# Performance work log

Hardware: AMD Instinct MI355X
Metric: run time of the kernel (lower is better)

## Reference

```python
import jax, jax.numpy as jnp
import numpy as np

N = 512           # nodes
DIM = 64          # feature dim (in_dim == dim)
KS = (0.9, 0.7, 0.6)
M_DIM = 17
EDGE_DIM = 1
EIN = 2 * DIM + 1 + EDGE_DIM  # EGNN edge-mlp input width = 130
L = 3             # shared EGNN layers per scale


def _rn(k, shape, s=0.05):
    return jax.random.normal(k, shape, jnp.float32) * s


def setup_inputs() -> dict:
    key = jax.random.key(0)
    k = jax.random.split(key, 12)
    feat = jax.random.normal(k[0], (1, N, DIM), jnp.float32)
    coor = jax.random.normal(k[1], (1, N, 3), jnp.float32)
    # sparse-ish binary adjacency stored densely, as the module expects
    edge = (jax.random.uniform(k[2], (1, N, N, 1)) < 0.05).astype(jnp.float32)
    return {
        "feat": feat, "coor": coor, "edge": edge,
        "We1": _rn(k[3], (L, EIN, 2 * EIN)), "be1": jnp.zeros((L, 2 * EIN), jnp.float32),
        "We2": _rn(k[4], (L, 2 * EIN, M_DIM)), "be2": jnp.zeros((L, M_DIM), jnp.float32),
        "Wc1": _rn(k[5], (L, M_DIM, 4 * M_DIM)), "bc1": jnp.zeros((L, 4 * M_DIM), jnp.float32),
        "Wc2": _rn(k[6], (L, 4 * M_DIM, 1)), "bc2": jnp.zeros((L, 1), jnp.float32),
        "Wn1": _rn(k[7], (L, DIM + M_DIM, 2 * DIM)), "bn1": jnp.zeros((L, 2 * DIM), jnp.float32),
        "Wn2": _rn(k[8], (L, 2 * DIM, DIM)), "bn2": jnp.zeros((L, DIM), jnp.float32),
        "wp": _rn(k[9], (len(KS), DIM)), "bp": jnp.zeros((len(KS),), jnp.float32),
        "ep": 0,
    }


def _egnn(feats, coors, edges, We1, be1, We2, be2, Wc1, bc1, Wc2, bc2,
          Wn1, bn1, Wn2, bn2):
    # feats [B,n,d], coors [B,n,3], edges [B,n,n,1]
    rel = coors[:, :, None, :] - coors[:, None, :, :]           # [B,n,n,3]
    dist = jnp.sum(rel * rel, axis=-1, keepdims=True)           # [B,n,n,1]
    B, n, d = feats.shape
    fi = jnp.broadcast_to(feats[:, :, None, :], (B, n, n, d))
    fj = jnp.broadcast_to(feats[:, None, :, :], (B, n, n, d))
    e_in = jnp.concatenate([fi, fj, dist, edges], axis=-1)      # [B,n,n,EIN]
    m = jax.nn.silu(jax.nn.silu(e_in @ We1 + be1) @ We2 + be2)  # [B,n,n,M]
    cw = jax.nn.silu(m @ Wc1 + bc1) @ Wc2 + bc2                 # [B,n,n,1]
    coors_out = coors + jnp.sum(cw * rel, axis=2)               # [B,n,3]
    m_i = jnp.sum(m, axis=2)                                    # [B,n,M]
    h = jax.nn.silu(jnp.concatenate([feats, m_i], axis=-1) @ Wn1 + bn1) @ Wn2 + bn2
    return feats + h, coors_out


def _forward(feat, coor, edge, We1, be1, We2, be2, Wc1, bc1, Wc2, bc2,
             Wn1, bn1, Wn2, bn2, wp, bp):
    org_h, org_g, org_c = feat[0], edge[0, :, :, 0], coor[0]
    n_nodes = org_h.shape[0]
    ug = (org_g != 0).astype(jnp.float32)
    ug2 = ((ug @ ug) != 0).astype(jnp.float32)  # 2-hop closure adjacency
    hs = []
    for i, kf in enumerate(KS):
        kcnt = max(2, int(kf * n_nodes))
        scores = jax.nn.sigmoid(org_h @ wp[i] + bp[i])          # [n]
        vals, idx = jax.lax.top_k(scores, kcnt)
        h = org_h[idx] * vals[:, None]                          # gather + scale
        g = ug2[idx][:, idx]                                    # row+col gather
        c = org_c[idx]
        hc, coors, edges = h[None], c[None], g[None, :, :, None]
        for j in range(3):
            ht, coors = _egnn(hc, coors, edges,
                              We1[j], be1[j], We2[j], be2[j],
                              Wc1[j], bc1[j], Wc2[j], bc2[j],
                              Wn1[j], bn1[j], Wn2[j], bn2[j])
            hc = jax.nn.relu(hc + ht)
        # unpool: zero-scatter back to original node set
        h_full = jnp.zeros((n_nodes, hc.shape[-1]), hc.dtype).at[idx].set(hc[0])
        hs.append(h_full)
    out = hs[-1]
    for h_i in hs:
        out = jnp.maximum(out, h_i)
    return out


def reference(feat, coor, edge, We1, be1, We2, be2, Wc1, bc1, Wc2, bc2,
              Wn1, bn1, Wn2, bn2, wp, bp, ep):
    return _forward(feat, coor, edge, We1, be1, We2, be2, Wc1, bc1, Wc2, bc2,
                    Wn1, bn1, Wn2, bn2, wp, bp)
```

## Files before the change

### kernel.cpp

```cpp
#include <hip/hip_runtime.h>
#include <hip/hip_bf16.h>

typedef unsigned long long u64;
typedef unsigned int u32;
typedef unsigned short u16;

#define NN   512
#define DIMF 64
#define E2   260
#define KPAD 272
#define MD   17
#define MH   68
#define NH1  128
#define K0   460
#define K1   358
#define K2   307
#define KT   1125
#define O1   460
#define O2   818
#define PADU 1152
#define AS   272
#define NT0  8
#define NT1  6
#define NT2  5
#define T0T   (K0*NT0)
#define T01T  (T0T + K1*NT1)
#define TTOT  (T01T + K2*NT2)
#define PBLK  ((TTOT+3)/4)
#define MSTR  40
#define WVLDS 5120

#define KNEG  (-1.4426950408889634f)
#define LN2N  (-0.6931471805599453f)

typedef __attribute__((ext_vector_type(8)))  short short8;
typedef __attribute__((ext_vector_type(16))) float f32x16;

union SF  { int4 i4; u16 us[8]; u32 w[4]; short8 v; };
union F4U { float4 v; float2 h[2]; float f[4]; u32 w[4]; };

__device__ __forceinline__ float fast_exp2(float x){
#if __has_builtin(__builtin_amdgcn_exp2f)
    return __builtin_amdgcn_exp2f(x);
#else
    return __expf(x * 0.6931471805599453f);
#endif
}
__device__ __forceinline__ float fast_rcp(float x){
#if __has_builtin(__builtin_amdgcn_rcpf)
    return __builtin_amdgcn_rcpf(x);
#else
    return __fdividef(1.0f, x);
#endif
}
__device__ __forceinline__ float silups(float q){
    return q * fast_rcp(1.0f + fast_exp2(q));
}
__device__ __forceinline__ float sigf(float x){
    return fast_rcp(1.0f + fast_exp2(x * KNEG));
}
__device__ __forceinline__ u16 bf16_rne(float f){
    u32 u = __float_as_uint(f);
    u += 0x7FFFu + ((u >> 16) & 1u);
    return (u16)(u >> 16);
}
__device__ __forceinline__ float bf16f(u16 h){
    return __uint_as_float(((u32)h) << 16);
}
__device__ __forceinline__ u32 pk_bf16(float x, float y){
    float2 f2; f2.x = x; f2.y = y;
    __hip_bfloat162 h = __float22bfloat162_rn(f2);
    union { __hip_bfloat162 b; u32 u; } cv; cv.b = h;
    return cv.u;
}
__device__ __forceinline__ void lgkm_wait(){
#if __has_builtin(__builtin_amdgcn_s_waitcnt)
    __builtin_amdgcn_s_waitcnt(0xC07F);
#endif
}
__device__ __forceinline__ float2 f2add(float2 a, float2 b){ return float2{a.x+b.x, a.y+b.y}; }
__device__ __forceinline__ float2 f2mul(float2 a, float2 b){ return float2{a.x*b.x, a.y*b.y}; }
__device__ __forceinline__ float2 f2fma(float2 a, float2 b, float2 c){
    return float2{fmaf(a.x,b.x,c.x), fmaf(a.y,b.y,c.y)};
}
__device__ __forceinline__ float2 sig2s(float2 q){
    float ex = fast_exp2(q.x), ey = fast_exp2(q.y);
    float2 den = f2add(float2{1.0f, 1.0f}, float2{ex, ey});
    float2 r; r.x = fast_rcp(den.x); r.y = fast_rcp(den.y);
    return f2mul(q, r);
}

__global__ __launch_bounds__(256) void k_pre(
    const float* __restrict__ edge, const float* __restrict__ feat,
    const float* __restrict__ wp, const float* __restrict__ bp,
    const float* __restrict__ We2, const float* __restrict__ Wc1,
    const float* __restrict__ We1, const float* __restrict__ be2,
    const float* __restrict__ bc1, const float* __restrict__ Wc2,
    u64* __restrict__ ugw, float* __restrict__ scores,
    u16* __restrict__ W2f, u16* __restrict__ Wc1f,
    float* __restrict__ wdP, float* __restrict__ weP, float* __restrict__ be2P,
    float* __restrict__ bc1P, float* __restrict__ Wc2P, u64* __restrict__ ug2w){
    int blk = blockIdx.x, t = threadIdx.x;
    if (blk < 128){
        int i = blk*4 + (t>>6); int lane = t&63;
        const float* row = edge + (size_t)i*NN;
        for (int w = 0; w < 8; w++){
            u64 m = __ballot(row[w*64+lane] != 0.0f);
            if (lane == 0) ugw[i*8+w] = m;
        }
        return;
    }
    if (blk < 134){
        int gid = (blk-128)*256 + t; if (gid >= 3*NN) return;
        int l = gid>>9, n = gid&511;
        const float4* fr = (const float4*)(feat + n*DIMF);
        const float4* wr = (const float4*)(wp + l*DIMF);
        float s = bp[l];
        for (int d = 0; d < 16; d++){
            float4 f = fr[d], w = wr[d];
            s = fmaf(f.x, w.x, s); s = fmaf(f.y, w.y, s);
            s = fmaf(f.z, w.z, s); s = fmaf(f.w, w.w, s);
        }
        scores[gid] = sigf(s);
        return;
    }
    int idx = (blk-134)*256 + t;
    if (idx < 52224){
        int e = idx&7, lane = (idx>>3)&63, hl = (idx>>9)&1, c = (idx>>10)%17, jl = idx/17408;
        int q = lane>>5, nn = lane&31;
        int k = c*16 + q*8 + e;
        float v = (k < E2 && nn < MD) ? We2[jl*E2*MD + k*MD + nn] : 0.0f;
        u16 hi = bf16_rne(v);
        W2f[idx] = hl ? bf16_rne(v - bf16f(hi)) : hi;
        return;
    }
    idx -= 52224;
    if (idx < 9216){
        int e = idx & 7, lane = (idx>>3)&63, c2 = (idx>>9)&1, T = (idx>>10)%3, jl = idx/3072;
        int q = lane>>5, nn = lane&31;
        int o = c2*16 + q*8 + e, h = T*32 + nn;
        float v = (o < MD && h < MH) ? Wc1[jl*MD*MH + o*MH + h] : 0.0f;
        Wc1f[idx] = bf16_rne(v);
        return;
    }
    idx -= 9216;
    if (idx < 816){ int jl = idx/KPAD, k = idx%KPAD;
        wdP[idx] = (k < E2) ? We1[jl*130*E2 + 128*E2 + k]*KNEG : 0.0f; return; }
    idx -= 816;
    if (idx < 816){ int jl = idx/KPAD, k = idx%KPAD;
        weP[idx] = (k < E2) ? We1[jl*130*E2 + 129*E2 + k]*KNEG : 0.0f; return; }
    idx -= 816;
    if (idx < 96){ int jl = idx/32, o = idx%32;
        be2P[idx] = (o < MD) ? be2[jl*MD+o]*KNEG : 0.0f; return; }
    idx -= 96;
    if (idx < 288){ int jl = idx/96, h = idx%96;
        bc1P[idx] = (h < MH) ? bc1[jl*MH+h]*KNEG : 0.0f; return; }
    idx -= 288;
    if (idx < 288){ int jl = idx/96, h = idx%96;
        Wc2P[idx] = (h < MH) ? Wc2[jl*MH+h]*LN2N : 0.0f; return; }
    idx -= 288;
    if (idx < 4096){ ug2w[idx] = 0ULL; return; }
}

__global__ __launch_bounds__(512) void k_sortug2(
    const float* __restrict__ scores, const u64* __restrict__ ugw,
    float* __restrict__ svals, int* __restrict__ sidx, int* __restrict__ rev,
    u64* __restrict__ ug2w){
    int blk = blockIdx.x, t = threadIdx.x;
    if (blk < 3){
        int l = blk;
        __shared__ float sk[NN];
        __shared__ int   si[NN];
        float key = scores[l*NN+t]; int idx = t;
        rev[l*NN+t] = -1;
        for (int k = 2; k <= NN; k <<= 1){
            for (int jj = k>>1; jj > 0; jj >>= 1){
                float kb; int ib;
                if (jj >= 64){
                    sk[t] = key; si[t] = idx;
                    __syncthreads();
                    kb = sk[t^jj]; ib = si[t^jj];
                    __syncthreads();
                } else {
                    kb = __shfl_xor(key, jj);
                    ib = __shfl_xor(idx, jj);
                }
                bool aFirst = (key > kb) || (key == kb && idx < ib);
                bool down   = ((t & k) == 0);
                bool lower  = ((t & jj) == 0);
                bool keep   = (aFirst == (lower == down));
                key = keep ? key : kb;
                idx = keep ? idx : ib;
            }
        }
        svals[l*NN+t] = key; sidx[l*NN+t] = idx;
        int kcnt = (l==0)?K0:(l==1)?K1:K2;
        if (t < kcnt) rev[l*NN + idx] = t;
    } else {
        int gid = (blk-3)*512 + t;
        int i  = gid >> 6;
        int w  = (gid >> 3) & 7;
        int kc = gid & 7;
        u64 rm = ugw[i*8 + kc];
        u64 acc = 0;
        int base = kc*64;
        while (rm){
            int k2 = __builtin_ctzll(rm);
            rm &= rm - 1;
            acc |= ugw[(base + k2)*8 + w];
        }
        if (acc) atomicOr(&ug2w[i*8 + w], acc);
    }
}

__device__ __forceinline__ void ab_comp(int jl, const float* __restrict__ We1,
                                        const float* __restrict__ be1, float hval,
                                        int u, int lane,
                                        float* __restrict__ Ap, float* __restrict__ BF){
    const float* W = We1 + jl*130*E2;
    int r  = 4*lane;
    int rt = 256 + lane;
    int rtc = (lane < 4) ? rt : 256;
    F4U av; av.v = *(const float4*)(be1 + jl*E2 + r);
    F4U bv; bv.f[0]=bv.f[1]=bv.f[2]=bv.f[3]=0.0f;
    float avx = be1[jl*E2 + rtc];
    float bvx = 0.0f;
    for (int d = 0; d < DIMF; d++){
        float hv = __shfl(hval, d);
        F4U w1; w1.v = *(const float4*)(W + d*E2 + r);
        F4U w2; w2.v = *(const float4*)(W + (DIMF+d)*E2 + r);
#pragma unroll
        for (int i = 0; i < 4; i++){
            av.f[i] = fmaf(hv, w1.f[i], av.f[i]);
            bv.f[i] = fmaf(hv, w2.f[i], bv.f[i]);
        }
        avx = fmaf(hv, W[d*E2 + rtc], avx);
        bvx = fmaf(hv, W[(DIMF+d)*E2 + rtc], bvx);
    }
#pragma unroll
    for (int i = 0; i < 4; i++){ av.f[i] *= KNEG; bv.f[i] *= KNEG; }
    avx *= KNEG; bvx *= KNEG;
    *(float4*)(Ap + u*AS + r) = av.v;
    *(float4*)(BF + ((size_t)(lane>>1)*PADU + u)*8 + (lane&1)*4) = bv.v;
    if (lane < 16){
        int k = 256 + lane;
        float aval = (lane < 4) ? avx : 0.0f;
        float bval = (lane < 4) ? bvx : 0.0f;
        Ap[u*AS + k] = aval;
        BF[((size_t)(k>>3)*PADU + u)*8 + (k&7)] = bval;
    }
}

__global__ __launch_bounds__(256) void k_gab(
    const float* __restrict__ feat, const float* __restrict__ coor,
    const float* __restrict__ svals, const int* __restrict__ sidx,
    const float* __restrict__ We1, const float* __restrict__ be1,
    float* __restrict__ hc, float* __restrict__ c0, float* __restrict__ c1,
    float* __restrict__ mi, float* __restrict__ Ap, float* __restrict__ BF){
    int t = threadIdx.x; int u = blockIdx.x*4 + (t>>6); if (u >= KT) return;
    int lane = t&63;
    int l = (u<K0)?0:(u<O2)?1:2;
    int a = u - ((l==0)?0:(l==1)?O1:O2);
    int org = sidx[l*NN+a];
    float val = svals[l*NN+a];
    float hval = feat[org*DIMF+lane]*val;
    hc[u*DIMF+lane] = hval;
    if (lane < 3){ float c = coor[org*3+lane]; c0[u*4+lane]=c; c1[u*4+lane]=c; }
    if (lane == 3){ c0[u*4+3]=0.0f; c1[u*4+3]=0.0f; }
    if (lane < 20) mi[u*20+lane] = 0.0f;
    ab_comp(0, We1, be1, hval, u, lane, Ap, BF);
}

template<int DOCW>
__global__ __launch_bounds__(256, 4) void k_pair(
    int jl,
    const float* __restrict__ Ap, const float* __restrict__ BF,
    const u16* __restrict__ W2f, const u16* __restrict__ Wc1f,
    const float* __restrict__ wdP, const float* __restrict__ weP,
    const float* __restrict__ be2P, const float* __restrict__ bc1P,
    const float* __restrict__ Wc2P, const float* __restrict__ bc2,
    const float* __restrict__ cin, float* __restrict__ cout,
    float* __restrict__ mi, const int* __restrict__ sidx,
    const u64* __restrict__ ug2w){
    __shared__ __align__(16) char sWK[4*WVLDS];
    __shared__ __align__(16) char sWD[1088];
    __shared__ __align__(16) char sWE[1088];
    int t = threadIdx.x;
    if (t < 68)       ((float4*)sWD)[t]    = *(const float4*)(wdP + jl*KPAD + 4*t);
    else if (t < 136) ((float4*)sWE)[t-68] = *(const float4*)(weP + jl*KPAD + 4*(t-68));
    int wid0 = blockIdx.x*4 + (t>>6);
    int lane = t&63, n = lane&31, q = lane>>5;
    bool dead = (wid0 >= TTOT);
    int wid = dead ? (TTOT-1) : wid0;
    int l, kl, off, a, tile;
    if (wid < T0T)       { l=0; kl=K0; off=0;  a = wid>>3; tile = wid&7; }
    else if (wid < T01T) { int w = wid-T0T;  l=1; kl=K1; off=O1; a = w/NT1; tile = w - a*NT1; }
    else                 { int w = wid-T01T; l=2; kl=K2; off=O2; a = w/NT2; tile = w - a*NT2; }
    int u = off + a;
    int b0 = tile*64 + n, b1 = b0 + 32;
    float act0 = (b0 < kl) ? 1.0f : 0.0f;
    float act1 = (b1 < kl) ? 1.0f : 0.0f;
    int b0c = min(b0, kl-1), b1c = min(b1, kl-1);
    int ub0 = off + b0c, ub1 = off + b1c;
    int ia  = sidx[l*NN+a];
    int ib0 = sidx[l*NN+b0c], ib1 = sidx[l*NN+b1c];
    float ef0 = act0 * (float)((ug2w[ia*8 + (ib0>>6)] >> (ib0&63)) & 1ULL);
    float ef1 = act1 * (float)((ug2w[ia*8 + (ib1>>6)] >> (ib1&63)) & 1ULL);
    F4U ca;  ca.v  = ((const float4*)cin)[u];
    F4U cb0; cb0.v = ((const float4*)cin)[ub0];
    F4U cb1; cb1.v = ((const float4*)cin)[ub1];
    float tx0 = ca.f[0]-cb0.f[0], ty0 = ca.f[1]-cb0.f[1], tz0 = ca.f[2]-cb0.f[2];
    float tx1 = ca.f[0]-cb1.f[0], ty1 = ca.f[1]-cb1.f[1], tz1 = ca.f[2]-cb1.f[2];
    float dd0 = tx0*tx0 + ty0*ty0 + tz0*tz0;
    float dd1 = tx1*tx1 + ty1*ty1 + tz1*tz1;

    char* myk = sWK + (t>>6)*WVLDS;
    {
        const float* Au = Ap + u*AS;
        ((float4*)myk)[lane] = *(const float4*)(Au + 4*lane);
        if (lane < 4) ((float4*)myk)[64+lane] = *(const float4*)(Au + 256 + 4*lane);
    }
    __syncthreads();

    const float* pB0 = BF + ((size_t)q*PADU + ub0)*8;
    const float* pB1 = BF + ((size_t)q*PADU + ub1)*8;
    const u16*   pW  = W2f + jl*17408 + lane*8;
    const char*  pA  = myk + q*32;
    const char*  pWD = sWD + q*32;
    const char*  pWE = sWE + q*32;

    f32x16 acc0, acc1;
#pragma unroll
    for (int r = 0; r < 16; r++){ acc0[r] = 0.0f; acc1[r] = 0.0f; }

    F4U nb0a, nb0b, nb1a, nb1b; SF nwh;
    nb0a.v = *(const float4*)(pB0);     nb0b.v = *(const float4*)(pB0 + 4);
    nb1a.v = *(const float4*)(pB1);     nb1b.v = *(const float4*)(pB1 + 4);
    nwh.i4 = *(const int4*)(pW);

    float2 DD0{dd0,dd0}, EF0{ef0,ef0}, DD1{dd1,dd1}, EF1{ef1,ef1};

    for (int c = 0; c < 17; c++){
        F4U b0a = nb0a, b0b = nb0b, b1a = nb1a, b1b = nb1b;
        SF  wh  = nwh;
        pB0 += 2*PADU*8; pB1 += 2*PADU*8; pW += 1024;
        if (c < 16){
            nb0a.v = *(const float4*)(pB0);     nb0b.v = *(const float4*)(pB0 + 4);
            nb1a.v = *(const float4*)(pB1);     nb1b.v = *(const float4*)(pB1 + 4);
            nwh.i4 = *(const int4*)(pW);
        }
        F4U a0, a1, w0, w1, e0, e1;
        a0.v = *(const float4*)(pA);       a1.v = *(const float4*)(pA + 16);
        w0.v = *(const float4*)(pWD);      w1.v = *(const float4*)(pWD + 16);
        e0.v = *(const float4*)(pWE);      e1.v = *(const float4*)(pWE + 16);
        pA += 64; pWD += 64; pWE += 64;

        SF shi0, shi1;
#pragma unroll
        for (int h = 0; h < 2; h++){
            float2 p00 = f2fma(EF0, e0.h[h], f2fma(DD0, w0.h[h], f2add(a0.h[h], b0a.h[h])));
            float2 p01 = f2fma(EF0, e1.h[h], f2fma(DD0, w1.h[h], f2add(a1.h[h], b0b.h[h])));
            float2 p10 = f2fma(EF1, e0.h[h], f2fma(DD1, w0.h[h], f2add(a0.h[h], b1a.h[h])));
            float2 p11 = f2fma(EF1, e1.h[h], f2fma(DD1, w1.h[h], f2add(a1.h[h], b1b.h[h])));
            float2 s00 = sig2s(p00), s01 = sig2s(p01);
            float2 s10 = sig2s(p10), s11 = sig2s(p11);
            shi0.w[h]   = pk_bf16(s00.x, s00.y);
            shi0.w[2+h] = pk_bf16(s01.x, s01.y);
            shi1.w[h]   = pk_bf16(s10.x, s10.y);
            shi1.w[2+h] = pk_bf16(s11.x, s11.y);
        }
        acc0 = __builtin_amdgcn_mfma_f32_32x32x16_bf16(shi0.v, wh.v, acc0, 0, 0, 0);
        acc1 = __builtin_amdgcn_mfma_f32_32x32x16_bf16(shi1.v, wh.v, acc1, 0, 0, 0);
    }

    float be2v = be2P[jl*32 + n];
    u16* mlds = (u16*)myk;
    float msum = 0.0f;
#pragma unroll
    for (int r = 0; r < 16; r++){
        int row = (r&3) + 8*(r>>2) + 4*q;
        float m0 = silups(acc0[r] + be2v);
        float m1 = silups(acc1[r] + be2v);
        m0 = (tile*64 + row      < kl) ? m0 : 0.0f;
        m1 = (tile*64 + 32 + row < kl) ? m1 : 0.0f;
        msum += m0 + m1;
        if (DOCW){
            mlds[row*MSTR + n]        = bf16_rne(m0);
            mlds[(row+32)*MSTR + n]   = bf16_rne(m1);
        }
    }
    msum += __shfl_xor(msum, 32);
    if (!dead && lane < MD) atomicAdd(&mi[u*20 + lane], msum * LN2N);

    if (DOCW){
        lgkm_wait();
        const char* mb = (const char*)mlds;
        float gx = 0.0f, gy = 0.0f, gz = 0.0f;
        float bc2v = bc2[jl];
#pragma unroll
        for (int S = 0; S < 2; S++){
            SF af0, af1;
            af0.i4 = *(const int4*)(mb + (S*32+n)*(MSTR*2) + q*16);
            af1.i4 = *(const int4*)(mb + (S*32+n)*(MSTR*2) + 32 + q*16);
            float cwp[16];
#pragma unroll
            for (int r = 0; r < 16; r++) cwp[r] = 0.0f;
            for (int T = 0; T < 3; T++){
                SF bb0, bb1;
                bb0.i4 = *(const int4*)(Wc1f + jl*3072 + T*1024 +       lane*8);
                bb1.i4 = *(const int4*)(Wc1f + jl*3072 + T*1024 + 512 + lane*8);
                f32x16 p2;
#pragma unroll
                for (int r = 0; r < 16; r++) p2[r] = 0.0f;
                p2 = __builtin_amdgcn_mfma_f32_32x32x16_bf16(af0.v, bb0.v, p2, 0, 0, 0);
                p2 = __builtin_amdgcn_mfma_f32_32x32x16_bf16(af1.v, bb1.v, p2, 0, 0, 0);
                float bc1v = bc1P[jl*96 + T*32 + n];
                float wc2v = Wc2P[jl*96 + T*32 + n];
#pragma unroll
                for (int r = 0; r < 16; r++)
                    cwp[r] = fmaf(silups(p2[r] + bc1v), wc2v, cwp[r]);
            }
#pragma unroll
            for (int r = 0; r < 16; r++){
                int row  = (r&3) + 8*(r>>2) + 4*q + S*32;
                int brow = tile*64 + row;
                F4U cbr; cbr.v = ((const float4*)cin)[off + min(brow, kl-1)];
                float cw = cwp[r] + ((n == 0) ? bc2v : 0.0f);
                cw = (brow < kl) ? cw : 0.0f;
                gx = fmaf(cw, ca.f[0]-cbr.f[0], gx);
                gy = fmaf(cw, ca.f[1]-cbr.f[1], gy);
                gz = fmaf(cw, ca.f[2]-cbr.f[2], gz);
            }
        }
#pragma unroll
        for (int s = 1; s < 64; s <<= 1){
            gx += __shfl_xor(gx, s); gy += __shfl_xor(gy, s); gz += __shfl_xor(gz, s);
        }
        if (!dead && lane == 0){
            atomicAdd(&cout[u*4+0], gx);
            atomicAdd(&cout[u*4+1], gy);
            atomicAdd(&cout[u*4+2], gz);
        }
    }
}

__global__ __launch_bounds__(256) void k_nodeab(
    int jl, int donext, int docopy,
    const float* __restrict__ Wn1, const float* __restrict__ bn1,
    const float* __restrict__ Wn2, const float* __restrict__ bn2,
    const float* __restrict__ We1, const float* __restrict__ be1,
    float* __restrict__ hc, float* __restrict__ mi,
    const float* __restrict__ ccur, float* __restrict__ cnext,
    float* __restrict__ Ap, float* __restrict__ BF){
    int t = threadIdx.x; int u = blockIdx.x*4 + (t>>6); if (u >= KT) return;
    int lane = t&63;
    float hval = hc[u*DIMF+lane];
    float mval = (lane < MD) ? mi[u*20+lane] : 0.0f;
    const float* W1 = Wn1 + jl*(DIMF+MD)*NH1;
    float v0 = bn1[jl*NH1+lane], v1 = bn1[jl*NH1+lane+64];
    for (int d = 0; d < DIMF; d++){
        float x = __shfl(hval, d);
        v0 = fmaf(x, W1[d*NH1+lane],    v0);
        v1 = fmaf(x, W1[d*NH1+lane+64], v1);
    }
    for (int d = 0; d < MD; d++){
        float x = __shfl(mval, d);
        v0 = fmaf(x, W1[(DIMF+d)*NH1+lane],    v0);
        v1 = fmaf(x, W1[(DIMF+d)*NH1+lane+64], v1);
    }
    float s0 = silups(v0 * KNEG) * LN2N, s1 = silups(v1 * KNEG) * LN2N;
    const float* W2 = Wn2 + jl*NH1*DIMF;
    float h = bn2[jl*DIMF+lane];
    for (int i = 0; i < 64; i++) h = fmaf(__shfl(s0, i), W2[i*DIMF+lane], h);
    for (int i = 0; i < 64; i++) h = fmaf(__shfl(s1, i), W2[(64+i)*DIMF+lane], h);
    float hn = fmaxf(0.0f, fmaf(2.0f, hval, h));
    hc[u*DIMF+lane] = hn;
    if (donext){
        if (lane < 20) mi[u*20+lane] = 0.0f;
        if (docopy && lane < 4) cnext[u*4+lane] = ccur[u*4+lane];
        ab_comp(jl+1, We1, be1, hn, u, lane, Ap, BF);
    }
}

__global__ void k_final(const float* __restrict__ hc, const int* __restrict__ rev,
                        float* __restrict__ out){
    int gid = blockIdx.x*blockDim.x + threadIdx.x;
    if (gid >= NN*DIMF) return;
    int nn = gid>>6, d = gid&63;
    float v = 0.0f;
    int a0 = rev[0*NN+nn]; if (a0 >= 0) v = fmaxf(v, hc[(0  + a0)*DIMF + d]);
    int a1 = rev[1*NN+nn]; if (a1 >= 0) v = fmaxf(v, hc[(O1 + a1)*DIMF + d]);
    int a2 = rev[2*NN+nn]; if (a2 >= 0) v = fmaxf(v, hc[(O2 + a2)*DIMF + d]);
    out[gid] = v;
}

extern "C" void kernel_launch(void* const* d_in, const int* in_sizes, int n_in,
                              void* d_out, int out_size, void* d_ws, size_t ws_size,
                              hipStream_t stream) {
    (void)in_sizes; (void)n_in; (void)out_size; (void)ws_size;
    const float* feat = (const float*)d_in[0];
    const float* coor = (const float*)d_in[1];
    const float* edge = (const float*)d_in[2];
    const float* We1  = (const float*)d_in[3];
    const float* be1  = (const float*)d_in[4];
    const float* We2  = (const float*)d_in[5];
    const float* be2  = (const float*)d_in[6];
    const float* Wc1  = (const float*)d_in[7];
    const float* bc1  = (const float*)d_in[8];
    const float* Wc2  = (const float*)d_in[9];
    const float* bc2  = (const float*)d_in[10];
    const float* Wn1  = (const float*)d_in[11];
    const float* bn1  = (const float*)d_in[12];
    const float* Wn2  = (const float*)d_in[13];
    const float* bn2  = (const float*)d_in[14];
    const float* wp   = (const float*)d_in[15];
    const float* bp   = (const float*)d_in[16];
    float* out = (float*)d_out;

    char* wsb = (char*)d_ws;
    u64*   ugw    = (u64*)  (wsb + 0);
    u64*   ug2w   = (u64*)  (wsb + 32768);
    float* scores = (float*)(wsb + 65536);
    float* svals  = (float*)(wsb + 71680);
    int*   sidx   = (int*)  (wsb + 77824);
    int*   rev    = (int*)  (wsb + 83968);
    float* c0     = (float*)(wsb + 90112);
    float* c1     = (float*)(wsb + 108544);
    float* mi     = (float*)(wsb + 126976);
    float* hc     = (float*)(wsb + 217088);
    float* Ap     = (float*)(wsb + 505344);
    float* BF     = (float*)(wsb + 1729536);
    u16*   W2f    = (u16*)  (wsb + 2982912);
    u16*   Wc1f   = (u16*)  (wsb + 3087360);
    float* wdP    = (float*)(wsb + 3105792);
    float* weP    = (float*)(wsb + 3109120);
    float* be2P   = (float*)(wsb + 3112448);
    float* bc1P   = (float*)(wsb + 3112832);
    float* Wc2P   = (float*)(wsb + 3113984);

    k_pre<<<399, 256, 0, stream>>>(edge, feat, wp, bp, We2, Wc1, We1, be2, bc1, Wc2,
                                   ugw, scores, W2f, Wc1f,
                                   wdP, weP, be2P, bc1P, Wc2P, ug2w);
    k_sortug2<<<67, 512, 0, stream>>>(scores, ugw, svals, sidx, rev, ug2w);
    k_gab<<<282, 256, 0, stream>>>(feat, coor, svals, sidx, We1, be1,
                                   hc, c0, c1, mi, Ap, BF);
    k_pair<1><<<PBLK, 256, 0, stream>>>(0, Ap, BF, W2f, Wc1f,
                                        wdP, weP, be2P, bc1P, Wc2P, bc2,
                                        c0, c1, mi, sidx, ug2w);
    k_nodeab<<<282, 256, 0, stream>>>(0, 1, 1, Wn1, bn1, Wn2, bn2, We1, be1,
                                      hc, mi, c1, c0, Ap, BF);
    k_pair<1><<<PBLK, 256, 0, stream>>>(1, Ap, BF, W2f, Wc1f,
                                        wdP, weP, be2P, bc1P, Wc2P, bc2,
                                        c1, c0, mi, sidx, ug2w);
    k_nodeab<<<282, 256, 0, stream>>>(1, 1, 0, Wn1, bn1, Wn2, bn2, We1, be1,
                                      hc, mi, c0, c1, Ap, BF);
    k_pair<0><<<PBLK, 256, 0, stream>>>(2, Ap, BF, W2f, Wc1f,
                                        wdP, weP, be2P, bc1P, Wc2P, bc2,
                                        c0, c1, mi, sidx, ug2w);
    k_nodeab<<<282, 256, 0, stream>>>(2, 0, 0, Wn1, bn1, Wn2, bn2, We1, be1,
                                      hc, mi, c0, c1, Ap, BF);
    k_final<<<128, 256, 0, stream>>>(hc, rev, out);
}
```

Baseline: 357.7 us.

## Fold edge-weight term into per-wave A row variants and fuse final max into node kernel

The pair kernel used to apply the binary edge feature through an extra FMA per element against a shared edge-weight vector. It now keeps two copies of the A row in LDS, one plain and one with the edge weights pre-added, and each column picks a copy by its edge bit. That removes a multiply-add and an LDS read stream per inner step, at the cost of twice the per-wave LDS footprint and an extra A read per column pair. Separately, the final max-unpool kernel is removed: the output is zeroed in k_pre and the last node kernel does an unsigned atomicMax into it, which is valid because post-ReLU values are non-negative.

New measurement: 347.5 us. 2.8% less time.

```diff
diff --git a/kernel.cpp b/kernel.cpp
--- a/kernel.cpp
+++ b/kernel.cpp
@@ -86,8 +86,8 @@
 __device__ __forceinline__ float2 sig2s(float2 q){
     float ex = fast_exp2(q.x), ey = fast_exp2(q.y);
     float2 den = f2add(float2{1.0f, 1.0f}, float2{ex, ey});
-    float2 r; r.x = fast_rcp(den.x); r.y = fast_rcp(den.y);
-    return f2mul(q, r);
+    float rx = fast_rcp(den.x), ry = fast_rcp(den.y);
+    return f2mul(q, float2{rx, ry});
 }
 
 __global__ __launch_bounds__(256) void k_pre(
@@ -99,7 +99,8 @@
     u64* __restrict__ ugw, float* __restrict__ scores,
     u16* __restrict__ W2f, u16* __restrict__ Wc1f,
     float* __restrict__ wdP, float* __restrict__ weP, float* __restrict__ be2P,
-    float* __restrict__ bc1P, float* __restrict__ Wc2P, u64* __restrict__ ug2w){
+    float* __restrict__ bc1P, float* __restrict__ Wc2P, u64* __restrict__ ug2w,
+    float* __restrict__ outz){
     int blk = blockIdx.x, t = threadIdx.x;
     if (blk < 128){
         int i = blk*4 + (t>>6); int lane = t&63;
@@ -160,6 +161,8 @@
         Wc2P[idx] = (h < MH) ? Wc2[jl*MH+h]*LN2N : 0.0f; return; }
     idx -= 288;
     if (idx < 4096){ ug2w[idx] = 0ULL; return; }
+    idx -= 4096;
+    if (idx < NN*DIMF){ outz[idx] = 0.0f; return; }
 }
 
 __global__ __launch_bounds__(512) void k_sortug2(
@@ -284,10 +287,8 @@
     const u64* __restrict__ ug2w){
     __shared__ __align__(16) char sWK[4*WVLDS];
     __shared__ __align__(16) char sWD[1088];
-    __shared__ __align__(16) char sWE[1088];
     int t = threadIdx.x;
-    if (t < 68)       ((float4*)sWD)[t]    = *(const float4*)(wdP + jl*KPAD + 4*t);
-    else if (t < 136) ((float4*)sWE)[t-68] = *(const float4*)(weP + jl*KPAD + 4*(t-68));
+    if (t < 68) ((float4*)sWD)[t] = *(const float4*)(wdP + jl*KPAD + 4*t);
     int wid0 = blockIdx.x*4 + (t>>6);
     int lane = t&63, n = lane&31, q = lane>>5;
     bool dead = (wid0 >= TTOT);
@@ -298,14 +299,14 @@
     else                 { int w = wid-T01T; l=2; kl=K2; off=O2; a = w/NT2; tile = w - a*NT2; }
     int u = off + a;
     int b0 = tile*64 + n, b1 = b0 + 32;
-    float act0 = (b0 < kl) ? 1.0f : 0.0f;
-    float act1 = (b1 < kl) ? 1.0f : 0.0f;
     int b0c = min(b0, kl-1), b1c = min(b1, kl-1);
     int ub0 = off + b0c, ub1 = off + b1c;
     int ia  = sidx[l*NN+a];
     int ib0 = sidx[l*NN+b0c], ib1 = sidx[l*NN+b1c];
-    float ef0 = act0 * (float)((ug2w[ia*8 + (ib0>>6)] >> (ib0&63)) & 1ULL);
-    float ef1 = act1 * (float)((ug2w[ia*8 + (ib1>>6)] >> (ib1&63)) & 1ULL);
+    int eb0 = (int)((ug2w[ia*8 + (ib0>>6)] >> (ib0&63)) & 1ULL);
+    int eb1 = (int)((ug2w[ia*8 + (ib1>>6)] >> (ib1&63)) & 1ULL);
+    int sel0 = (b0 < kl) ? eb0 : 0;
+    int sel1 = (b1 < kl) ? eb1 : 0;
     F4U ca;  ca.v  = ((const float4*)cin)[u];
     F4U cb0; cb0.v = ((const float4*)cin)[ub0];
     F4U cb1; cb1.v = ((const float4*)cin)[ub1];
@@ -317,17 +318,32 @@
     char* myk = sWK + (t>>6)*WVLDS;
     {
         const float* Au = Ap + u*AS;
-        ((float4*)myk)[lane] = *(const float4*)(Au + 4*lane);
-        if (lane < 4) ((float4*)myk)[64+lane] = *(const float4*)(Au + 256 + 4*lane);
+        const float* Ew = weP + jl*KPAD;
+        F4U av; av.v = *(const float4*)(Au + 4*lane);
+        F4U ev; ev.v = *(const float4*)(Ew + 4*lane);
+        ((float4*)myk)[lane] = av.v;
+        F4U sv;
+#pragma unroll
+        for (int i = 0; i < 4; i++) sv.f[i] = av.f[i] + ev.f[i];
+        ((float4*)(myk + 1088))[lane] = sv.v;
+        if (lane < 4){
+            F4U at; at.v = *(const float4*)(Au + 256 + 4*lane);
+            F4U et; et.v = *(const float4*)(Ew + 256 + 4*lane);
+            ((float4*)myk)[64+lane] = at.v;
+            F4U st;
+#pragma unroll
+            for (int i = 0; i < 4; i++) st.f[i] = at.f[i] + et.f[i];
+            ((float4*)(myk + 1088))[64+lane] = st.v;
+        }
     }
     __syncthreads();
 
     const float* pB0 = BF + ((size_t)q*PADU + ub0)*8;
     const float* pB1 = BF + ((size_t)q*PADU + ub1)*8;
     const u16*   pW  = W2f + jl*17408 + lane*8;
-    const char*  pA  = myk + q*32;
+    const char*  pA0 = myk + sel0*1088 + q*32;
+    const char*  pA1 = myk + sel1*1088 + q*32;
     const char*  pWD = sWD + q*32;
-    const char*  pWE = sWE + q*32;
 
     f32x16 acc0, acc1;
 #pragma unroll
@@ -338,7 +354,7 @@
     nb1a.v = *(const float4*)(pB1);     nb1b.v = *(const float4*)(pB1 + 4);
     nwh.i4 = *(const int4*)(pW);
 
-    float2 DD0{dd0,dd0}, EF0{ef0,ef0}, DD1{dd1,dd1}, EF1{ef1,ef1};
+    float2 DD0{dd0,dd0}, DD1{dd1,dd1};
 
     for (int c = 0; c < 17; c++){
         F4U b0a = nb0a, b0b = nb0b, b1a = nb1a, b1b = nb1b;
@@ -349,19 +365,19 @@
             nb1a.v = *(const float4*)(pB1);     nb1b.v = *(const float4*)(pB1 + 4);
             nwh.i4 = *(const int4*)(pW);
         }
-        F4U a0, a1, w0, w1, e0, e1;
-        a0.v = *(const float4*)(pA);       a1.v = *(const float4*)(pA + 16);
-        w0.v = *(const float4*)(pWD);      w1.v = *(const float4*)(pWD + 16);
-        e0.v = *(const float4*)(pWE);      e1.v = *(const float4*)(pWE + 16);
-        pA += 64; pWD += 64; pWE += 64;
+        F4U a00, a01, a10, a11, w0, w1;
+        a00.v = *(const float4*)(pA0);     a01.v = *(const float4*)(pA0 + 16);
+        a10.v = *(const float4*)(pA1);     a11.v = *(const float4*)(pA1 + 16);
+        w0.v  = *(const float4*)(pWD);     w1.v  = *(const float4*)(pWD + 16);
+        pA0 += 64; pA1 += 64; pWD += 64;
 
         SF shi0, shi1;
 #pragma unroll
         for (int h = 0; h < 2; h++){
-            float2 p00 = f2fma(EF0, e0.h[h], f2fma(DD0, w0.h[h], f2add(a0.h[h], b0a.h[h])));
-            float2 p01 = f2fma(EF0, e1.h[h], f2fma(DD0, w1.h[h], f2add(a1.h[h], b0b.h[h])));
-            float2 p10 = f2fma(EF1, e0.h[h], f2fma(DD1, w0.h[h], f2add(a0.h[h], b1a.h[h])));
-            float2 p11 = f2fma(EF1, e1.h[h], f2fma(DD1, w1.h[h], f2add(a1.h[h], b1b.h[h])));
+            float2 p00 = f2fma(DD0, w0.h[h], f2add(a00.h[h], b0a.h[h]));
+            float2 p01 = f2fma(DD0, w1.h[h], f2add(a01.h[h], b0b.h[h]));
+            float2 p10 = f2fma(DD1, w0.h[h], f2add(a10.h[h], b1a.h[h]));
+            float2 p11 = f2fma(DD1, w1.h[h], f2add(a11.h[h], b1b.h[h]));
             float2 s00 = sig2s(p00), s01 = sig2s(p01);
             float2 s10 = sig2s(p10), s11 = sig2s(p11);
             shi0.w[h]   = pk_bf16(s00.x, s00.y);
@@ -451,7 +467,8 @@
     const float* __restrict__ We1, const float* __restrict__ be1,
     float* __restrict__ hc, float* __restrict__ mi,
     const float* __restrict__ ccur, float* __restrict__ cnext,
-    float* __restrict__ Ap, float* __restrict__ BF){
+    float* __restrict__ Ap, float* __restrict__ BF,
+    const int* __restrict__ sidx, float* __restrict__ outv){
     int t = threadIdx.x; int u = blockIdx.x*4 + (t>>6); if (u >= KT) return;
     int lane = t&63;
     float hval = hc[u*DIMF+lane];
@@ -479,19 +496,12 @@
         if (lane < 20) mi[u*20+lane] = 0.0f;
         if (docopy && lane < 4) cnext[u*4+lane] = ccur[u*4+lane];
         ab_comp(jl+1, We1, be1, hn, u, lane, Ap, BF);
-    }
-}
-
-__global__ void k_final(const float* __restrict__ hc, const int* __restrict__ rev,
-                        float* __restrict__ out){
-    int gid = blockIdx.x*blockDim.x + threadIdx.x;
-    if (gid >= NN*DIMF) return;
-    int nn = gid>>6, d = gid&63;
-    float v = 0.0f;
-    int a0 = rev[0*NN+nn]; if (a0 >= 0) v = fmaxf(v, hc[(0  + a0)*DIMF + d]);
-    int a1 = rev[1*NN+nn]; if (a1 >= 0) v = fmaxf(v, hc[(O1 + a1)*DIMF + d]);
-    int a2 = rev[2*NN+nn]; if (a2 >= 0) v = fmaxf(v, hc[(O2 + a2)*DIMF + d]);
-    out[gid] = v;
+    } else {
+        int l2 = (u<K0)?0:(u<O2)?1:2;
+        int a2 = u - ((l2==0)?0:(l2==1)?O1:O2);
+        int org = sidx[l2*NN+a2];
+        atomicMax((u32*)&outv[org*DIMF+lane], __float_as_uint(hn));
+    }
 }
 
 extern "C" void kernel_launch(void* const* d_in, const int* in_sizes, int n_in,
@@ -538,9 +548,9 @@
     float* bc1P   = (float*)(wsb + 3112832);
     float* Wc2P   = (float*)(wsb + 3113984);
 
-    k_pre<<<399, 256, 0, stream>>>(edge, feat, wp, bp, We2, Wc1, We1, be2, bc1, Wc2,
+    k_pre<<<527, 256, 0, stream>>>(edge, feat, wp, bp, We2, Wc1, We1, be2, bc1, Wc2,
                                    ugw, scores, W2f, Wc1f,
-                                   wdP, weP, be2P, bc1P, Wc2P, ug2w);
+                                   wdP, weP, be2P, bc1P, Wc2P, ug2w, out);
     k_sortug2<<<67, 512, 0, stream>>>(scores, ugw, svals, sidx, rev, ug2w);
     k_gab<<<282, 256, 0, stream>>>(feat, coor, svals, sidx, We1, be1,
                                    hc, c0, c1, mi, Ap, BF);
@@ -548,16 +558,15 @@
                                         wdP, weP, be2P, bc1P, Wc2P, bc2,
                                         c0, c1, mi, sidx, ug2w);
     k_nodeab<<<282, 256, 0, stream>>>(0, 1, 1, Wn1, bn1, Wn2, bn2, We1, be1,
-                                      hc, mi, c1, c0, Ap, BF);
+                                      hc, mi, c1, c0, Ap, BF, sidx, out);
     k_pair<1><<<PBLK, 256, 0, stream>>>(1, Ap, BF, W2f, Wc1f,
                                         wdP, weP, be2P, bc1P, Wc2P, bc2,
                                         c1, c0, mi, sidx, ug2w);
     k_nodeab<<<282, 256, 0, stream>>>(1, 1, 0, Wn1, bn1, Wn2, bn2, We1, be1,
-                                      hc, mi, c0, c1, Ap, BF);
+                                      hc, mi, c0, c1, Ap, BF, sidx, out);
     k_pair<0><<<PBLK, 256, 0, stream>>>(2, Ap, BF, W2f, Wc1f,
                                         wdP, weP, be2P, bc1P, Wc2P, bc2,
                                         c0, c1, mi, sidx, ug2w);
     k_nodeab<<<282, 256, 0, stream>>>(2, 0, 0, Wn1, bn1, Wn2, bn2, We1, be1,
-                                      hc, mi, c0, c1, Ap, BF);
-    k_final<<<128, 256, 0, stream>>>(hc, rev, out);
-}
+                                      hc, mi, c0, c1, Ap, BF, sidx, out);
+}
```
